# Performance work log

Hardware: AMD Instinct MI355X
Metric: run time of the kernel (lower is better)

## Reference

```python
import jax, jax.numpy as jnp
import numpy as np

N = 100000      # nodes
E = 1600000     # edges
D_IN = 256
D_HID = 256
D_OUT = 256
DROP_P = 0.5


def setup_inputs() -> dict:
    key = jax.random.key(0)
    ks = jax.random.split(key, 10)
    s = 1.0 / np.sqrt(D_HID)
    return {
        "z": jax.random.normal(ks[0], (N, D_OUT), jnp.float32),
        "omega": jax.random.normal(ks[1], (N, D_IN), jnp.float32),
        "edge_index": jax.random.randint(ks[2], (2, E), 0, N, jnp.int32),
        "W_lin": jax.random.normal(ks[3], (D_IN, D_HID), jnp.float32) * s,
        "b_lin": jnp.zeros((D_HID,), jnp.float32),
        "W_g1": jax.random.normal(ks[4], (D_HID, D_HID), jnp.float32) * s,
        "b_g1": jnp.zeros((D_HID,), jnp.float32),
        "W_g2": jax.random.normal(ks[5], (D_HID, D_OUT), jnp.float32) * s,
        "b_g2": jnp.zeros((D_OUT,), jnp.float32),
        "mask1": jax.random.bernoulli(ks[6], 1.0 - DROP_P, (N, D_HID)),
        "mask2": jax.random.bernoulli(ks[7], 1.0 - DROP_P, (N, D_HID)),
    }


def _gcn_norm(edge_index):
    # add self-loops, symmetric normalization deg^-1/2 * deg^-1/2
    loop = jnp.arange(N, dtype=edge_index.dtype)
    src = jnp.concatenate([edge_index[0], loop])
    dst = jnp.concatenate([edge_index[1], loop])
    deg = jax.ops.segment_sum(jnp.ones_like(dst, jnp.float32), dst, num_segments=N)
    dinv = jax.lax.rsqrt(deg)  # deg >= 1 because of self-loops
    norm = dinv[src] * dinv[dst]  # [E+N]
    return src, dst, norm


def _gcn_conv(x, W, b, src, dst, norm):
    h = x @ W                                  # [N, d_out]
    msg = h[src] * norm[:, None]               # gather over edges
    out = jax.ops.segment_sum(msg, dst, num_segments=N)  # scatter-add
    return out + b


def _dropout(x, mask):
    return jnp.where(mask, x * (1.0 / (1.0 - DROP_P)), 0.0)


def reference(z, omega, edge_index, W_lin, b_lin, W_g1, b_g1, W_g2, b_g2, mask1, mask2):
    src, dst, norm = _gcn_norm(edge_index)
    # layer 0: Linear + relu + dropout
    h = _dropout(jax.nn.relu(omega @ W_lin + b_lin), mask1)
    # layer 1: GCNConv + relu + dropout
    h = _dropout(jax.nn.relu(_gcn_conv(h, W_g1, b_g1, src, dst, norm)), mask2)
    # layer 2: GCNConv
    h = _gcn_conv(h, W_g2, b_g2, src, dst, norm)
    return z * h
```

## Files before the change

kernel.cpp:

```cpp
#include <hip/hip_runtime.h>
#include <stdint.h>

#define NN 100000
#define EE 1600000
#define DD 256
#define GB0 1563
#define NCNT 1024
#define NSUB 128

typedef __bf16 bf16;
typedef __attribute__((ext_vector_type(8))) __bf16 bf16x8;
typedef __attribute__((ext_vector_type(4))) float f32x4;
typedef __attribute__((ext_vector_type(4))) unsigned int u32x4;
typedef __attribute__((ext_vector_type(8))) unsigned short u16x8;

typedef __attribute__((address_space(1))) const unsigned int g_u32c;
typedef __attribute__((address_space(3))) unsigned int lds_u32;

__device__ __forceinline__ float bflo(unsigned int u) {
    union { unsigned int u; float f; } x; x.u = u << 16; return x.f;
}
__device__ __forceinline__ float bfhi(unsigned int u) {
    union { unsigned int u; float f; } x; x.u = u & 0xFFFF0000u; return x.f;
}
__device__ __forceinline__ unsigned short f2bf(float f) {
    return __builtin_bit_cast(unsigned short, (__bf16)f);
}

__global__ void dinv_k(const int* __restrict__ cnt, float* __restrict__ dinv) {
    int i = blockIdx.x * 256 + threadIdx.x;
    if (i < NN) dinv[i] = rsqrtf((float)(cnt[i] + 1));
}

__global__ __launch_bounds__(256) void prep_k(
    const float* __restrict__ W0, const float* __restrict__ W1, const float* __restrict__ W2,
    bf16* __restrict__ T0, bf16* __restrict__ T1, bf16* __restrict__ T2,
    const unsigned int* __restrict__ m, int* __restrict__ flag) {
    int b = blockIdx.x;
    if (b == 192) {
        if (threadIdx.x < 64) {
            unsigned int v = m[threadIdx.x];
            int bad = (v > 1u && v != 0x3F800000u) ? 1 : 0;
            unsigned long long bl = __ballot(bad);
            if (threadIdx.x == 0) *flag = (bl != 0ull) ? 1 : 0;
        }
        return;
    }
    const float* W = b < 64 ? W0 : (b < 128 ? W1 : W2);
    bf16*       T  = b < 64 ? T0 : (b < 128 ? T1 : T2);
    int bb = b & 63;
    __shared__ float tile[32][33];
    int bx = bb & 7, by = bb >> 3;
    int tx = threadIdx.x & 31, ty = threadIdx.x >> 5;
    #pragma unroll
    for (int r = 0; r < 32; r += 8)
        tile[ty + r][tx] = W[(size_t)(by * 32 + ty + r) * DD + bx * 32 + tx];
    __syncthreads();
    #pragma unroll
    for (int r = 0; r < 32; r += 8)
        T[(size_t)(bx * 32 + ty + r) * DD + by * 32 + tx] = (bf16)tile[tx][ty + r];
}

template <int EPI, int F32A>
__device__ __forceinline__ void gemm_body(
    const void* __restrict__ Ap, const bf16* __restrict__ Wt,
    const float* __restrict__ bias, const void* __restrict__ mask,
    const int* __restrict__ flagp, const float* __restrict__ z,
    void* __restrict__ outp, bf16* As, bf16* Bs, int m0) {
    int tid = threadIdx.x;
    int wid = tid >> 6, lane = tid & 63;
    int lr = lane & 15, lk = lane >> 4;
    int rx = lr & 7;

    f32x4 acc[4][4] = {};

    for (int k0 = 0; k0 < DD; k0 += 64) {
        #pragma unroll
        for (int i = 0; i < 2; i++) {
            int f = i * 256 + tid;
            int row = f >> 3;
            int cl  = f & 7;
            int cg  = cl ^ (row & 7);
            int gr = m0 + row; if (gr > NN - 1) gr = NN - 1;
            if (F32A) {
                const float* sp = (const float*)Ap + (size_t)gr * DD + k0 + cl * 8;
                float4 v0 = *(const float4*)sp;
                float4 v1 = *(const float4*)(sp + 4);
                u16x8 o = { f2bf(v0.x), f2bf(v0.y), f2bf(v0.z), f2bf(v0.w),
                            f2bf(v1.x), f2bf(v1.y), f2bf(v1.z), f2bf(v1.w) };
                *(u16x8*)(As + row * 64 + cg * 8) = o;
            } else {
                __builtin_amdgcn_global_load_lds(
                    (g_u32c*)((const bf16*)Ap + (size_t)gr * DD + k0 + cg * 8),
                    (lds_u32*)(As + (size_t)f * 8), 16, 0, 0);
            }
        }
        #pragma unroll
        for (int i = 0; i < 8; i++) {
            int f = i * 256 + tid;
            int row = f >> 3;
            int cg  = (f & 7) ^ (row & 7);
            __builtin_amdgcn_global_load_lds(
                (g_u32c*)(Wt + (size_t)row * DD + k0 + cg * 8),
                (lds_u32*)(Bs + (size_t)f * 8), 16, 0, 0);
        }
        __syncthreads();
        #pragma unroll
        for (int kk = 0; kk < 2; kk++) {
            bf16x8 af[4], bfr[4];
            #pragma unroll
            for (int mi = 0; mi < 4; mi++)
                af[mi] = *(const bf16x8*)(As + (mi * 16 + lr) * 64 + (((kk * 4 + lk) ^ rx) * 8));
            #pragma unroll
            for (int ni = 0; ni < 4; ni++)
                bfr[ni] = *(const bf16x8*)(Bs + (wid * 64 + ni * 16 + lr) * 64 + (((kk * 4 + lk) ^ rx) * 8));
            #pragma unroll
            for (int mi = 0; mi < 4; mi++)
                #pragma unroll
                for (int ni = 0; ni < 4; ni++)
                    acc[mi][ni] = __builtin_amdgcn_mfma_f32_16x16x32_bf16(
                        bfr[ni], af[mi], acc[mi][ni], 0, 0, 0);
        }
        __syncthreads();
    }

    int bm = (EPI == 1) ? *flagp : 0;
    #pragma unroll
    for (int mi = 0; mi < 4; mi++) {
        int gr = m0 + mi * 16 + lr;
        if (gr >= NN) continue;
        #pragma unroll
        for (int ni = 0; ni < 4; ni++) {
            int gc = wid * 64 + ni * 16 + lk * 4;
            size_t idx = (size_t)gr * DD + gc;
            float4 b4 = *(const float4*)(bias + gc);
            float v0 = acc[mi][ni][0] + b4.x;
            float v1 = acc[mi][ni][1] + b4.y;
            float v2 = acc[mi][ni][2] + b4.z;
            float v3 = acc[mi][ni][3] + b4.w;
            if (EPI == 1) {
                v0 = fmaxf(v0, 0.f); v1 = fmaxf(v1, 0.f);
                v2 = fmaxf(v2, 0.f); v3 = fmaxf(v3, 0.f);
                if (bm) {
                    uchar4 u = *(const uchar4*)((const unsigned char*)mask + idx);
                    v0 *= u.x ? 2.f : 0.f; v1 *= u.y ? 2.f : 0.f;
                    v2 *= u.z ? 2.f : 0.f; v3 *= u.w ? 2.f : 0.f;
                } else {
                    uint4 u = *(const uint4*)((const unsigned int*)mask + idx);
                    v0 *= u.x ? 2.f : 0.f; v1 *= u.y ? 2.f : 0.f;
                    v2 *= u.z ? 2.f : 0.f; v3 *= u.w ? 2.f : 0.f;
                }
                ushort4 o = { f2bf(v0), f2bf(v1), f2bf(v2), f2bf(v3) };
                *(ushort4*)((unsigned short*)outp + idx) = o;
            } else {
                f32x4 zz = __builtin_nontemporal_load((const f32x4*)(z + idx));
                f32x4 o = { v0 * zz.x, v1 * zz.y, v2 * zz.z, v3 * zz.w };
                __builtin_nontemporal_store(o, (f32x4*)((float*)outp + idx));
            }
        }
    }
}

__global__ __launch_bounds__(256) void g0fill_k(
    const float* __restrict__ omega, const bf16* __restrict__ Wt,
    const float* __restrict__ bias, const void* __restrict__ mask,
    const int* __restrict__ flagp, bf16* __restrict__ outp,
    const int* __restrict__ src, const int* __restrict__ dst,
    int* __restrict__ cnt, int* __restrict__ cs) {
    __shared__ __align__(16) bf16 As[64 * 64];
    __shared__ __align__(16) bf16 Bs[256 * 64];
    int b = blockIdx.x;
    if (b < NCNT) {
        int prt = b & 7;
        int sub = b >> 3;
        int lo = prt * (NN >> 3);
        int hi = (prt == 7) ? NN : lo + (NN >> 3);
        const int per = EE / NSUB;
        int e0 = sub * per;
        int e1 = (sub == NSUB - 1) ? EE : e0 + per;
        for (int e = e0 + threadIdx.x; e < e1; e += 256) {
            int d = dst[e];
            if (d >= lo && d < hi) {
                int s = src[e];
                int slot = atomicAdd(&cnt[d], 1);
                if (slot < 64) cs[(d << 6) + slot] = s;
            }
        }
        return;
    }
    gemm_body<1, 1>(omega, Wt, bias, mask, flagp, nullptr, outp, As, Bs,
                    (b - NCNT) * 64);
}

template <int ID, int EPI>
__global__ __launch_bounds__(256) void gemm_k(
    const bf16* __restrict__ Ap, const bf16* __restrict__ Wt,
    const float* __restrict__ bias, const void* __restrict__ mask,
    const int* __restrict__ flagp, const float* __restrict__ z,
    void* __restrict__ outp) {
    __shared__ __align__(16) bf16 As[64 * 64];
    __shared__ __align__(16) bf16 Bs[256 * 64];
    int m0 = blockIdx.x * 64;
    if (m0 >= NN) return;
    gemm_body<EPI, 0>(Ap, Wt, bias, mask, flagp, z, outp, As, Bs, m0);
}

#define AGG_GET(J, UVAR, MVAR)                                                   \
    {                                                                            \
        int _i = 2 * (J) + half;                                                 \
        int _s = __shfl(sl, _i & 63);                                            \
        float _w = __shfl(wl, _i & 63);                                          \
        MVAR = (_i < nume) ? _w : 0.f;                                           \
        UVAR = *(const u32x4*)(tb + (((size_t)(unsigned)_s) << 9) + lcoff);      \
    }
#define AGG_FMA(UVAR, MVAR)                                                      \
    {                                                                            \
        acc[0] = fmaf(MVAR, bflo(UVAR.x), acc[0]);                               \
        acc[1] = fmaf(MVAR, bfhi(UVAR.x), acc[1]);                               \
        acc[2] = fmaf(MVAR, bflo(UVAR.y), acc[2]);                               \
        acc[3] = fmaf(MVAR, bfhi(UVAR.y), acc[3]);                               \
        acc[4] = fmaf(MVAR, bflo(UVAR.z), acc[4]);                               \
        acc[5] = fmaf(MVAR, bfhi(UVAR.z), acc[5]);                               \
        acc[6] = fmaf(MVAR, bflo(UVAR.w), acc[6]);                               \
        acc[7] = fmaf(MVAR, bfhi(UVAR.w), acc[7]);                               \
    }

__global__ __launch_bounds__(256) void agg_k(
    const bf16* __restrict__ t, const int* __restrict__ cnt,
    const int* __restrict__ cs, const float* __restrict__ dinv,
    bf16* __restrict__ out) {
    int node = blockIdx.x * 4 + (threadIdx.x >> 6);
    if (node >= NN) return;
    int lane = threadIdx.x & 63;
    int half = lane >> 5;
    int lc = lane & 31;
    int nume = cnt[node];
    if (nume > 63) nume = 63;

    float acc[8] = {};
    const char* tb = (const char*)t;
    size_t lcoff = (size_t)(lc << 4);

    if (nume > 0) {
        int base = node << 6;
        int sl = 0; float wl = 0.f;
        if (lane < nume) {
            sl = __builtin_nontemporal_load(cs + base + lane);
            wl = dinv[sl];
        }
        int nit = (nume + 1) >> 1;

        u32x4 ua, ub, uc, ud;
        float ma, mb, mc, md;
        AGG_GET(0, ua, ma);
        AGG_GET(1, ub, mb);
        AGG_GET(2, uc, mc);
        int j = 0;
        for (; j + 3 < nit; j += 4) {
            AGG_GET(j + 3, ud, md); AGG_FMA(ua, ma);
            AGG_GET(j + 4, ua, ma); AGG_FMA(ub, mb);
            AGG_GET(j + 5, ub, mb); AGG_FMA(uc, mc);
            AGG_GET(j + 6, uc, mc); AGG_FMA(ud, md);
        }
        int rem = nit - j;
        if (rem > 0) AGG_FMA(ua, ma);
        if (rem > 1) AGG_FMA(ub, mb);
        if (rem > 2) AGG_FMA(uc, mc);
    }

    float dn = dinv[node];
    #pragma unroll
    for (int i = 0; i < 8; i++) acc[i] += __shfl_xor(acc[i], 32);
    if (half == 0) {
        u32x4 u = *(const u32x4*)(tb + (((size_t)(unsigned)node) << 9) + lcoff);
        acc[0] = fmaf(dn, bflo(u.x), acc[0]);
        acc[1] = fmaf(dn, bfhi(u.x), acc[1]);
        acc[2] = fmaf(dn, bflo(u.y), acc[2]);
        acc[3] = fmaf(dn, bfhi(u.y), acc[3]);
        acc[4] = fmaf(dn, bflo(u.z), acc[4]);
        acc[5] = fmaf(dn, bfhi(u.z), acc[5]);
        acc[6] = fmaf(dn, bflo(u.w), acc[6]);
        acc[7] = fmaf(dn, bfhi(u.w), acc[7]);
        #pragma unroll
        for (int i = 0; i < 8; i++) acc[i] *= dn;
        u16x8 o = { f2bf(acc[0]), f2bf(acc[1]), f2bf(acc[2]), f2bf(acc[3]),
                    f2bf(acc[4]), f2bf(acc[5]), f2bf(acc[6]), f2bf(acc[7]) };
        __builtin_nontemporal_store(o, (u16x8*)((unsigned short*)out + (size_t)node * DD + lc * 8));
    }
}

extern "C" void kernel_launch(void* const* d_in, const int* in_sizes, int n_in,
                              void* d_out, int out_size, void* d_ws, size_t ws_size,
                              hipStream_t stream) {
    const float* z     = (const float*)d_in[0];
    const float* omega = (const float*)d_in[1];
    const int*   eidx  = (const int*)d_in[2];
    const float* W_lin = (const float*)d_in[3];
    const float* b_lin = (const float*)d_in[4];
    const float* W_g1  = (const float*)d_in[5];
    const float* b_g1  = (const float*)d_in[6];
    const float* W_g2  = (const float*)d_in[7];
    const float* b_g2  = (const float*)d_in[8];
    const void*  mask1 = d_in[9];
    const void*  mask2 = d_in[10];

    const int* e_src = eidx;
    const int* e_dst = eidx + EE;

    char* p = (char*)d_ws;
    size_t off = 0;
    auto alloc = [&](size_t bytes) -> char* {
        char* r = p + off;
        off = (off + bytes + 255) & ~(size_t)255;
        return r;
    };
    const int NB256 = (NN + 255) / 256;
    int*   flag = (int*)  alloc(4);
    int*   cnt  = (int*)  alloc((size_t)NN * 4);
    float* dinv = (float*)alloc((size_t)NN * 4);
    int*   cs   = (int*)  alloc((size_t)NN * 64 * 4);
    bf16*  WtL  = (bf16*) alloc((size_t)DD * DD * 2);
    bf16*  Wt1  = (bf16*) alloc((size_t)DD * DD * 2);
    bf16*  Wt2  = (bf16*) alloc((size_t)DD * DD * 2);
    const size_t NBH = (size_t)NN * DD * 2;
    bf16*  S1   = (bf16*) alloc(NBH);
    bf16*  S2   = (bf16*) alloc(NBH);

    (void)hipMemsetAsync(cnt, 0, (size_t)NN * 4, stream);
    prep_k<<<193, 256, 0, stream>>>(W_lin, W_g1, W_g2, WtL, Wt1, Wt2,
                                    (const unsigned int*)mask1, flag);

    g0fill_k<<<NCNT + GB0, 256, 0, stream>>>(omega, WtL, b_lin, mask1, flag,
                                             S1, e_src, e_dst, cnt, cs);
    dinv_k<<<NB256, 256, 0, stream>>>(cnt, dinv);

    agg_k<<<NN / 4, 256, 0, stream>>>(S1, cnt, cs, dinv, S2);
    gemm_k<1, 1><<<GB0, 256, 0, stream>>>(S2, Wt1, b_g1, mask2, flag, nullptr, S1);
    agg_k<<<NN / 4, 256, 0, stream>>>(S1, cnt, cs, dinv, S2);
    gemm_k<2, 2><<<GB0, 256, 0, stream>>>(S2, Wt2, b_g2, nullptr, flag, z, d_out);
}
```

Measured before the change: 555.5 us.

## Move edge fill into weight-prep kernel and compute dinv inline in aggregation

The edge bucketing (count plus adjacency fill) moves out of the first GEMM kernel into the weight-transpose prep kernel, so the first GEMM runs as its own launch. The separate dinv kernel and its buffer are removed, and the aggregation computes rsqrt(cnt+1) on the fly for the node and each neighbour. This drops one launch and one pass over the degree array. In exchange the atomic fill no longer overlaps with the first GEMM, and each aggregation recomputes rsqrt from gathered counts.

Measured after the change: 552.8 us (median of 2 runs). No clear change (-0.5%).

```diff
diff --git a/kernel.cpp b/kernel.cpp
--- a/kernel.cpp
+++ b/kernel.cpp
@@ -5,7 +5,7 @@
 #define EE 1600000
 #define DD 256
 #define GB0 1563
-#define NCNT 1024
+#define NFILL 1024
 #define NSUB 128
 
 typedef __bf16 bf16;
@@ -27,16 +27,33 @@
     return __builtin_bit_cast(unsigned short, (__bf16)f);
 }
 
-__global__ void dinv_k(const int* __restrict__ cnt, float* __restrict__ dinv) {
-    int i = blockIdx.x * 256 + threadIdx.x;
-    if (i < NN) dinv[i] = rsqrtf((float)(cnt[i] + 1));
-}
-
-__global__ __launch_bounds__(256) void prep_k(
-    const float* __restrict__ W0, const float* __restrict__ W1, const float* __restrict__ W2,
-    bf16* __restrict__ T0, bf16* __restrict__ T1, bf16* __restrict__ T2,
+__global__ __launch_bounds__(256) void fillprep_k(
+    const int* __restrict__ src, const int* __restrict__ dst,
+    int* __restrict__ cnt, int* __restrict__ cs,
+    const float* __restrict__ W0, const float* __restrict__ W1,
+    const float* __restrict__ W2, bf16* __restrict__ T0,
+    bf16* __restrict__ T1, bf16* __restrict__ T2,
     const unsigned int* __restrict__ m, int* __restrict__ flag) {
     int b = blockIdx.x;
+    if (b < NFILL) {
+        int prt = b & 7;
+        int sub = b >> 3;
+        int lo = prt * (NN >> 3);
+        int hi = (prt == 7) ? NN : lo + (NN >> 3);
+        const int per = EE / NSUB;
+        int e0 = sub * per;
+        int e1 = (sub == NSUB - 1) ? EE : e0 + per;
+        for (int e = e0 + threadIdx.x; e < e1; e += 256) {
+            int d = dst[e];
+            if (d >= lo && d < hi) {
+                int s = src[e];
+                int slot = atomicAdd(&cnt[d], 1);
+                if (slot < 64) cs[(d << 6) + slot] = s;
+            }
+        }
+        return;
+    }
+    b -= NFILL;
     if (b == 192) {
         if (threadIdx.x < 64) {
             unsigned int v = m[threadIdx.x];
@@ -161,35 +178,15 @@
     }
 }
 
-__global__ __launch_bounds__(256) void g0fill_k(
+__global__ __launch_bounds__(256) void gemm0_k(
     const float* __restrict__ omega, const bf16* __restrict__ Wt,
     const float* __restrict__ bias, const void* __restrict__ mask,
-    const int* __restrict__ flagp, bf16* __restrict__ outp,
-    const int* __restrict__ src, const int* __restrict__ dst,
-    int* __restrict__ cnt, int* __restrict__ cs) {
+    const int* __restrict__ flagp, bf16* __restrict__ outp) {
     __shared__ __align__(16) bf16 As[64 * 64];
     __shared__ __align__(16) bf16 Bs[256 * 64];
-    int b = blockIdx.x;
-    if (b < NCNT) {
-        int prt = b & 7;
-        int sub = b >> 3;
-        int lo = prt * (NN >> 3);
-        int hi = (prt == 7) ? NN : lo + (NN >> 3);
-        const int per = EE / NSUB;
-        int e0 = sub * per;
-        int e1 = (sub == NSUB - 1) ? EE : e0 + per;
-        for (int e = e0 + threadIdx.x; e < e1; e += 256) {
-            int d = dst[e];
-            if (d >= lo && d < hi) {
-                int s = src[e];
-                int slot = atomicAdd(&cnt[d], 1);
-                if (slot < 64) cs[(d << 6) + slot] = s;
-            }
-        }
-        return;
-    }
-    gemm_body<1, 1>(omega, Wt, bias, mask, flagp, nullptr, outp, As, Bs,
-                    (b - NCNT) * 64);
+    int m0 = blockIdx.x * 64;
+    if (m0 >= NN) return;
+    gemm_body<1, 1>(omega, Wt, bias, mask, flagp, nullptr, outp, As, Bs, m0);
 }
 
 template <int ID, int EPI>
@@ -227,15 +224,14 @@
 
 __global__ __launch_bounds__(256) void agg_k(
     const bf16* __restrict__ t, const int* __restrict__ cnt,
-    const int* __restrict__ cs, const float* __restrict__ dinv,
-    bf16* __restrict__ out) {
+    const int* __restrict__ cs, bf16* __restrict__ out) {
     int node = blockIdx.x * 4 + (threadIdx.x >> 6);
     if (node >= NN) return;
     int lane = threadIdx.x & 63;
     int half = lane >> 5;
     int lc = lane & 31;
-    int nume = cnt[node];
-    if (nume > 63) nume = 63;
+    int cn = cnt[node];
+    int nume = cn > 63 ? 63 : cn;
 
     float acc[8] = {};
     const char* tb = (const char*)t;
@@ -246,7 +242,7 @@
         int sl = 0; float wl = 0.f;
         if (lane < nume) {
             sl = __builtin_nontemporal_load(cs + base + lane);
-            wl = dinv[sl];
+            wl = rsqrtf((float)(cnt[sl] + 1));
         }
         int nit = (nume + 1) >> 1;
 
@@ -268,7 +264,7 @@
         if (rem > 2) AGG_FMA(uc, mc);
     }
 
-    float dn = dinv[node];
+    float dn = rsqrtf((float)(cn + 1));
     #pragma unroll
     for (int i = 0; i < 8; i++) acc[i] += __shfl_xor(acc[i], 32);
     if (half == 0) {
@@ -314,10 +310,8 @@
         off = (off + bytes + 255) & ~(size_t)255;
         return r;
     };
-    const int NB256 = (NN + 255) / 256;
     int*   flag = (int*)  alloc(4);
     int*   cnt  = (int*)  alloc((size_t)NN * 4);
-    float* dinv = (float*)alloc((size_t)NN * 4);
     int*   cs   = (int*)  alloc((size_t)NN * 64 * 4);
     bf16*  WtL  = (bf16*) alloc((size_t)DD * DD * 2);
     bf16*  Wt1  = (bf16*) alloc((size_t)DD * DD * 2);
@@ -327,15 +321,13 @@
     bf16*  S2   = (bf16*) alloc(NBH);
 
     (void)hipMemsetAsync(cnt, 0, (size_t)NN * 4, stream);
-    prep_k<<<193, 256, 0, stream>>>(W_lin, W_g1, W_g2, WtL, Wt1, Wt2,
-                                    (const unsigned int*)mask1, flag);
-
-    g0fill_k<<<NCNT + GB0, 256, 0, stream>>>(omega, WtL, b_lin, mask1, flag,
-                                             S1, e_src, e_dst, cnt, cs);
-    dinv_k<<<NB256, 256, 0, stream>>>(cnt, dinv);
-
-    agg_k<<<NN / 4, 256, 0, stream>>>(S1, cnt, cs, dinv, S2);
+    fillprep_k<<<NFILL + 193, 256, 0, stream>>>(e_src, e_dst, cnt, cs,
+                                                W_lin, W_g1, W_g2, WtL, Wt1, Wt2,
+                                                (const unsigned int*)mask1, flag);
+
+    gemm0_k<<<GB0, 256, 0, stream>>>(omega, WtL, b_lin, mask1, flag, S1);
+    agg_k<<<NN / 4, 256, 0, stream>>>(S1, cnt, cs, S2);
     gemm_k<1, 1><<<GB0, 256, 0, stream>>>(S2, Wt1, b_g1, mask2, flag, nullptr, S1);
-    agg_k<<<NN / 4, 256, 0, stream>>>(S1, cnt, cs, dinv, S2);
+    agg_k<<<NN / 4, 256, 0, stream>>>(S1, cnt, cs, S2);
     gemm_k<2, 2><<<GB0, 256, 0, stream>>>(S2, Wt2, b_g2, nullptr, flag, z, d_out);
 }
```
